# Kernel optimization log

Measured on AMD Instinct MI355X. Metric: run time of the kernel, lower is better.

## Reference

```python
import jax, jax.numpy as jnp
import numpy as np


def setup_inputs() -> dict:
    key = jax.random.key(0)
    k1, k2 = jax.random.split(key)
    B, N, C, H, W = 8, 16, 4, 128, 256
    preds = jax.random.normal(k1, (B, N, C, H, W), dtype=jnp.float32)
    gt = jax.random.normal(k2, (B, C, H, W), dtype=jnp.float32)
    return {"preds": preds, "gt": gt}


def reference(preds, gt):
    # preds: [B, N, C, H, W], gt: [B, C, H, W]
    N = preds.shape[1]
    # term1: mean over ensemble of |pred - obs|  -> [B, C, H, W]
    term1 = jnp.abs(preds - gt[:, None]).mean(axis=1)
    if N > 1:
        # pairwise |p_i - p_j| summed over i,j (diagonal is zero anyway)
        pairwise = jnp.abs(preds[:, :, None] - preds[:, None, :])  # [B,N,N,C,H,W]
        term2 = pairwise.sum(axis=(1, 2)) / (2 * N * (N - 1))
    else:
        term2 = jnp.zeros_like(term1)
    crps_field = term1 - term2
    return crps_field.mean()
```

## Files before the change

### kernel.cpp

```cpp
#include <hip/hip_runtime.h>


#define CHW      131072
#define CHW4     32768
#define NENS     16
#define BATCH    8
#define NPOINTS  (BATCH * CHW)
#define NP4      (NPOINTS / 4)
#define BLOCK    256
#define GRID1    (NP4 / BLOCK)

__global__ __launch_bounds__(BLOCK) void crps_partial_kernel(
    const float4* __restrict__ preds,
    const float4* __restrict__ gt,
    float* __restrict__ partial)
{
    const int t  = blockIdx.x * BLOCK + threadIdx.x;
    const int b  = t >> 15;
    const int s4 = t & (CHW4 - 1);

    const float4* pbase = preds + ((b * NENS) << 15) + s4;
    const float4 g = gt[t];

    float4 p[NENS];
#pragma unroll
    for (int n = 0; n < NENS; ++n)
        p[n] = pbase[n << 15];

    float a1 = 0.0f;
    float a2 = 0.0f;
#pragma unroll
    for (int i = 0; i < NENS; ++i) {
        a1 += fabsf(p[i].x - g.x) + fabsf(p[i].y - g.y)
            + fabsf(p[i].z - g.z) + fabsf(p[i].w - g.w);
#pragma unroll
        for (int j = i + 1; j < NENS; ++j) {
            a2 += fabsf(p[i].x - p[j].x) + fabsf(p[i].y - p[j].y)
                + fabsf(p[i].z - p[j].z) + fabsf(p[i].w - p[j].w);
        }
    }
    float local = a1 * (1.0f / 16.0f) - a2 * (1.0f / 240.0f);

#pragma unroll
    for (int off = 32; off > 0; off >>= 1)
        local += __shfl_down(local, off, 64);

    __shared__ float smem[BLOCK / 64];
    const int lane = threadIdx.x & 63;
    const int wid  = threadIdx.x >> 6;
    if (lane == 0) smem[wid] = local;
    __syncthreads();
    if (threadIdx.x == 0) {
        float s = 0.0f;
#pragma unroll
        for (int w = 0; w < BLOCK / 64; ++w) s += smem[w];
        partial[blockIdx.x] = s;
    }
}

__global__ __launch_bounds__(BLOCK) void crps_final_kernel(
    const float* __restrict__ partial, float* __restrict__ out)
{
    float local = 0.0f;
    for (int i = threadIdx.x; i < GRID1; i += BLOCK)
        local += partial[i];
#pragma unroll
    for (int off = 32; off > 0; off >>= 1)
        local += __shfl_down(local, off, 64);

    __shared__ float smem[BLOCK / 64];
    const int lane = threadIdx.x & 63;
    const int wid  = threadIdx.x >> 6;
    if (lane == 0) smem[wid] = local;
    __syncthreads();
    if (threadIdx.x == 0) {
        float s = 0.0f;
#pragma unroll
        for (int w = 0; w < BLOCK / 64; ++w) s += smem[w];
        out[0] = s * (1.0f / (float)NPOINTS);
    }
}

extern "C" void kernel_launch(void* const* d_in, const int* in_sizes, int n_in,
                              void* d_out, int out_size, void* d_ws, size_t ws_size,
                              hipStream_t stream) {
    const float4* preds = (const float4*)d_in[0];
    const float4* gt    = (const float4*)d_in[1];
    float* partial      = (float*)d_ws;
    float* out          = (float*)d_out;

    crps_partial_kernel<<<GRID1, BLOCK, 0, stream>>>(preds, gt, partial);
    crps_final_kernel<<<1, BLOCK, 0, stream>>>(partial, out);
}
```

Before: 94.06 us.

## Replace pairwise ensemble differences with sorting network and weighted rank sum

Replaces the O(N^2) pairwise absolute-difference sum with a Batcher odd-even merge sorting network of 63 comparators per component, followed by a weighted sum of sorted values (weights 2k-15). This cuts per-element ALU work from 120 abs-diff pairs to 63 min/max pairs plus 16 FMAs, aimed at a kernel that may be compute-bound on VALU. It keeps the result mathematically equivalent, but the summation order changes and the register shuffling in the network could add register pressure.

```diff
diff --git a/kernel.cpp b/kernel.cpp
--- a/kernel.cpp
+++ b/kernel.cpp
@@ -9,6 +9,29 @@
 #define NP4      (NPOINTS / 4)
 #define BLOCK    256
 #define GRID1    (NP4 / BLOCK)
+
+struct Net { int a[64]; int b[64]; int cnt; };
+constexpr Net make_net() {
+    Net nt{}; int c = 0; const int n = NENS;
+    for (int p = 1; p < n; p <<= 1)
+        for (int k = p; k >= 1; k >>= 1)
+            for (int j = k % p; j + k < n; j += 2 * k)
+                for (int i = 0; i < k && i + j + k < n; ++i)
+                    if ((i + j) / (2 * p) == (i + j + k) / (2 * p)) {
+                        nt.a[c] = i + j; nt.b[c] = i + j + k; ++c;
+                    }
+    nt.cnt = c;
+    return nt;
+}
+constexpr Net NET = make_net();
+static_assert(make_net().cnt == 63, "Batcher n=16 must have 63 comparators");
+
+__device__ __forceinline__ float4 f4min(float4 u, float4 v) {
+    return make_float4(fminf(u.x, v.x), fminf(u.y, v.y), fminf(u.z, v.z), fminf(u.w, v.w));
+}
+__device__ __forceinline__ float4 f4max(float4 u, float4 v) {
+    return make_float4(fmaxf(u.x, v.x), fmaxf(u.y, v.y), fmaxf(u.z, v.z), fmaxf(u.w, v.w));
+}
 
 __global__ __launch_bounds__(BLOCK) void crps_partial_kernel(
     const float4* __restrict__ preds,
@@ -27,19 +50,35 @@
     for (int n = 0; n < NENS; ++n)
         p[n] = pbase[n << 15];
 
-    float a1 = 0.0f;
-    float a2 = 0.0f;
+    float4 t1 = make_float4(0.f, 0.f, 0.f, 0.f);
 #pragma unroll
     for (int i = 0; i < NENS; ++i) {
-        a1 += fabsf(p[i].x - g.x) + fabsf(p[i].y - g.y)
-            + fabsf(p[i].z - g.z) + fabsf(p[i].w - g.w);
+        t1.x += fabsf(p[i].x - g.x);
+        t1.y += fabsf(p[i].y - g.y);
+        t1.z += fabsf(p[i].z - g.z);
+        t1.w += fabsf(p[i].w - g.w);
+    }
+
 #pragma unroll
-        for (int j = i + 1; j < NENS; ++j) {
-            a2 += fabsf(p[i].x - p[j].x) + fabsf(p[i].y - p[j].y)
-                + fabsf(p[i].z - p[j].z) + fabsf(p[i].w - p[j].w);
-        }
+    for (int c = 0; c < 63; ++c) {
+        const int ia = NET.a[c], ib = NET.b[c];
+        const float4 lo = f4min(p[ia], p[ib]);
+        const float4 hi = f4max(p[ia], p[ib]);
+        p[ia] = lo; p[ib] = hi;
     }
-    float local = a1 * (1.0f / 16.0f) - a2 * (1.0f / 240.0f);
+
+    float4 t2 = make_float4(0.f, 0.f, 0.f, 0.f);
+#pragma unroll
+    for (int k = 0; k < NENS; ++k) {
+        const float w = (float)(2 * k - 15);
+        t2.x = fmaf(w, p[k].x, t2.x);
+        t2.y = fmaf(w, p[k].y, t2.y);
+        t2.z = fmaf(w, p[k].z, t2.z);
+        t2.w = fmaf(w, p[k].w, t2.w);
+    }
+
+    float local = (t1.x + t1.y + t1.z + t1.w) * (1.0f / 16.0f)
+                - (t2.x + t2.y + t2.z + t2.w) * (1.0f / 240.0f);
 
 #pragma unroll
     for (int off = 32; off > 0; off >>= 1)
```

New measurement: 94.56 us. Within noise of the previous version (+0.5%).
